# Performance work log

Measured on AMD Instinct MI355X. Metric: run time of the kernel, lower is better.

Reference implementation:

```python
import jax, jax.numpy as jnp
import numpy as np

NUM_HEADS = 16
NUM_KV_HEADS = 8
HEAD_DIM = 128
ROPE_THETA = 10000.0
SOFTCAP = 50.0


def rotate_half(x):
    x1, x2 = jnp.split(x, 2, axis=-1)
    return jnp.concatenate((-x2, x1), axis=-1)


def rope_cos_sin(seq_len):
    inv_freq = 1.0 / (ROPE_THETA ** (jnp.arange(0, HEAD_DIM, 2, dtype=jnp.float32) / HEAD_DIM))
    t = jnp.arange(seq_len, dtype=jnp.float32)
    freqs = t[:, None] * inv_freq[None, :]          # [S, D/2]
    emb = jnp.concatenate((freqs, freqs), axis=-1)  # [S, D]
    return jnp.cos(emb), jnp.sin(emb)


def setup_inputs() -> dict:
    key = jax.random.key(0)
    k1, k2, k3, k4, k5 = jax.random.split(key, 5)
    B, S, H = 2, 2048, 2048
    sc = 1.0 / np.sqrt(H)
    return {
        "hidden_states": jax.random.normal(k1, (B, S, H), dtype=jnp.float32),
        "Wq": jax.random.normal(k2, (H, NUM_HEADS * HEAD_DIM), dtype=jnp.float32) * sc,
        "Wk": jax.random.normal(k3, (H, NUM_KV_HEADS * HEAD_DIM), dtype=jnp.float32) * sc,
        "Wv": jax.random.normal(k4, (H, NUM_KV_HEADS * HEAD_DIM), dtype=jnp.float32) * sc,
        "Wo": jax.random.normal(k5, (NUM_HEADS * HEAD_DIM, H), dtype=jnp.float32) * sc,
    }


def reference(hidden_states, Wq, Wk, Wv, Wo):
    B, S, _ = hidden_states.shape
    groups = NUM_HEADS // NUM_KV_HEADS

    # projections -> [B, heads, S, D]
    q = (hidden_states @ Wq).reshape(B, S, NUM_HEADS, HEAD_DIM).transpose(0, 2, 1, 3)
    k = (hidden_states @ Wk).reshape(B, S, NUM_KV_HEADS, HEAD_DIM).transpose(0, 2, 1, 3)
    v = (hidden_states @ Wv).reshape(B, S, NUM_KV_HEADS, HEAD_DIM).transpose(0, 2, 1, 3)

    cos, sin = rope_cos_sin(S)  # [S, D], broadcast over (B, heads)
    q = q * cos + rotate_half(q) * sin
    k = k * cos + rotate_half(k) * sin

    # GQA: expand KV heads (repeat_interleave along head dim)
    k = jnp.repeat(k, groups, axis=1)
    v = jnp.repeat(v, groups, axis=1)

    scores = jnp.einsum('bhsd,bhtd->bhst', q, k) / np.sqrt(HEAD_DIM)
    scores = jnp.tanh(scores / SOFTCAP) * SOFTCAP  # Gemma logit softcapping
    weights = jax.nn.softmax(scores.astype(jnp.float32), axis=-1).astype(q.dtype)

    out = jnp.einsum('bhst,bhtd->bhsd', weights, v)
    out = out.transpose(0, 2, 1, 3).reshape(B, S, NUM_HEADS * HEAD_DIM)
    return out @ Wo
```

## Files before the change

### kernel.cpp

```cpp
#include <hip/hip_runtime.h>
#include <math.h>

typedef __bf16 bf16;
typedef __bf16 bf16x8 __attribute__((ext_vector_type(8)));
typedef __bf16 bf16x4 __attribute__((ext_vector_type(4)));
typedef float f32x2 __attribute__((ext_vector_type(2)));
typedef float f32x4 __attribute__((ext_vector_type(4)));
typedef float f32x16 __attribute__((ext_vector_type(16)));
typedef unsigned int uint;
typedef uint u32x4 __attribute__((ext_vector_type(4)));
typedef uint u32x2 __attribute__((ext_vector_type(2)));
typedef __bf16 bf16x8_a __attribute__((ext_vector_type(8), __may_alias__));
typedef uint u32x2_a __attribute__((ext_vector_type(2), __may_alias__));
typedef __bf16 bf16x4_a __attribute__((ext_vector_type(4), __may_alias__));
typedef __bf16 bf16_a __attribute__((__may_alias__));

constexpr int BATCH = 2;
constexpr int SEQ   = 2048;
constexpr int HID   = 2048;
constexpr int NHEAD = 16;
constexpr int NKV   = 8;
constexpr int HD    = 128;
constexpr int MROWS = BATCH * SEQ;

#define DEVINL __device__ __forceinline__

#define BAR()                                 \
  do {                                        \
    asm volatile("" ::: "memory");            \
    __builtin_amdgcn_s_barrier();             \
    asm volatile("" ::: "memory");            \
  } while (0)

#define WAITV(N) asm volatile("s_waitcnt vmcnt(" #N ")" ::: "memory")

DEVINL void async16(void* l, const void* g) {
  __builtin_amdgcn_global_load_lds((const __attribute__((address_space(1))) void*)g,
                                   (__attribute__((address_space(3))) void*)l, 16, 0, 0);
}

DEVINL f32x4 mfma16(bf16x8 a, bf16x8 b, f32x4 c) {
  return __builtin_amdgcn_mfma_f32_16x16x32_bf16(a, b, c, 0, 0, 0);
}
DEVINL f32x16 mfma32(bf16x8 a, bf16x8 b, f32x16 c) {
  return __builtin_amdgcn_mfma_f32_32x32x16_bf16(a, b, c, 0, 0, 0);
}

DEVINL f32x4 fzero4() { f32x4 z; z[0] = 0.f; z[1] = 0.f; z[2] = 0.f; z[3] = 0.f; return z; }

DEVINL float ex2(float x) {
#if __has_builtin(__builtin_amdgcn_exp2f)
  return __builtin_amdgcn_exp2f(x);
#else
  return __expf(x * 0.6931471805599453f);
#endif
}

DEVINL uint pkbf16(float lo, float hi) {
  unsigned short l = __builtin_bit_cast(unsigned short, (bf16)lo);
  unsigned short h = __builtin_bit_cast(unsigned short, (bf16)hi);
  return (uint)l | ((uint)h << 16);
}

DEVINL u32x2 pswap(uint a, uint b) {
#if __has_builtin(__builtin_amdgcn_permlane32_swap)
  return __builtin_amdgcn_permlane32_swap(a, b, false, false);
#else
  int hl = (int)((threadIdx.x >> 5) & 1);
  uint as = __shfl_xor(a, 32), bs = __shfl_xor(b, 32);
  u32x2 r;
  r[0] = hl ? bs : a;
  r[1] = hl ? b : as;
  return r;
#endif
}

__global__ __launch_bounds__(256) void prep(const float* __restrict__ X,
                                            const float* __restrict__ Wq,
                                            const float* __restrict__ Wk,
                                            const float* __restrict__ Wv,
                                            const float* __restrict__ Wo,
                                            bf16* __restrict__ Xb,
                                            bf16* __restrict__ WqT, bf16* __restrict__ WkT,
                                            bf16* __restrict__ WvT, bf16* __restrict__ WoT,
                                            float* __restrict__ ct, float* __restrict__ st) {
  const int tid = threadIdx.x;
  const int z = blockIdx.z;
  if (z == 4) {
    int idx = (blockIdx.y * 32 + blockIdx.x) * 256 + tid;
    if (idx < SEQ * 64) {
      int s = idx >> 6, d = idx & 63;
      float freq = powf(10000.0f, -(float)d * (1.0f / 64.0f));
      float a = (float)s * freq;
      ct[idx] = cosf(a);
      st[idx] = sinf(a);
    }
    return;
  }
  if (z == 5) {
    int j = (blockIdx.y * 32 + blockIdx.x) * 256 + tid;
#pragma unroll
    for (int it = 0; it < 8; it++) {
      int e = (it * 262144 + j) * 4;
      float4 v = *(const float4*)(X + e);
      bf16x4 o;
      o[0] = (bf16)v.x; o[1] = (bf16)v.y; o[2] = (bf16)v.z; o[3] = (bf16)v.w;
      *(bf16x4*)(Xb + e) = o;
    }
    return;
  }
  __shared__ bf16 t[64][65];
  const float* W; bf16* WT; int N;
  switch (z) {
    case 0: W = Wq; WT = WqT; N = 2048; break;
    case 1: W = Wk; WT = WkT; N = 1024; break;
    case 2: W = Wv; WT = WvT; N = 1024; break;
    default: W = Wo; WT = WoT; N = 2048; break;
  }
  int n0 = blockIdx.x * 64, k0 = blockIdx.y * 64;
  if (n0 >= N) return;
#pragma unroll
  for (int p = 0; p < 4; p++) {
    int r = (tid >> 4) + p * 16;
    int c4 = (tid & 15) * 4;
    float4 v = *(const float4*)(&W[(size_t)(k0 + r) * N + n0 + c4]);
    t[r][c4 + 0] = (bf16)v.x;
    t[r][c4 + 1] = (bf16)v.y;
    t[r][c4 + 2] = (bf16)v.z;
    t[r][c4 + 3] = (bf16)v.w;
  }
  __syncthreads();
#pragma unroll
  for (int p = 0; p < 4; p++) {
    int nr = (tid >> 4) + p * 16;
    int kb = (tid & 15) * 4;
    bf16x4 o;
    o[0] = t[kb + 0][nr];
    o[1] = t[kb + 1][nr];
    o[2] = t[kb + 2][nr];
    o[3] = t[kb + 3][nr];
    *(bf16x4_a*)(&WT[(size_t)(n0 + nr) * 2048 + k0 + kb]) = o;
  }
}

__global__ __launch_bounds__(256) void vtrans(const bf16* __restrict__ V, bf16* __restrict__ VT) {
  __shared__ bf16 t[64][65];
  int s0 = blockIdx.x * 64, d0 = blockIdx.y * 64;
  int bh = blockIdx.z, b = bh >> 3, kvh = bh & 7;
  for (int i = threadIdx.x; i < 4096; i += 256) {
    int r = i >> 6, c = i & 63;
    t[r][c] = V[(size_t)(b * SEQ + s0 + r) * (NKV * HD) + kvh * HD + d0 + c];
  }
  __syncthreads();
  for (int i = threadIdx.x; i < 4096; i += 256) {
    int r = i >> 6, c = i & 63;
    VT[((size_t)bh * HD + d0 + r) * SEQ + s0 + c] = t[c][r];
  }
}

__global__ __launch_bounds__(256) void gemmA(const bf16* __restrict__ A,
                                             const bf16* __restrict__ BT,
                                             bf16* __restrict__ C0, bf16* __restrict__ C1,
                                             bf16* __restrict__ C2, int K,
                                             const float* __restrict__ ct,
                                             const float* __restrict__ st) {
  __shared__ alignas(16) char ldsA[16384];
  __shared__ alignas(16) char ldsB[16384];
  const int tid = threadIdx.x, lane = tid & 63, w = tid >> 6;
  const int l15 = lane & 15, l4 = lane >> 4;
  const int gx = 32;
  const int nwg = gx * gridDim.y;
  int id = blockIdx.y * gx + blockIdx.x;
  id = (id & 7) * (nwg >> 3) + (id >> 3);
  const int row0 = (id / gx) * 128;
  const int col0 = (id % gx) * 128;

  f32x4 acc[2][8];
#pragma unroll
  for (int mt = 0; mt < 2; mt++)
#pragma unroll
    for (int nt = 0; nt < 8; nt++) acc[mt][nt] = fzero4();

  const bf16* Asrc = A + (size_t)row0 * K;
  const bf16* Bsrc = BT + (size_t)col0 * K;
  const int nk = K >> 6;

  for (int t = 0; t < nk; ++t) {
    const int k0 = t << 6;
    BAR();
#pragma unroll
    for (int j = 0; j < 4; j++) {
      int ci = j * 256 + tid;
      int r = ci >> 3, ps = ci & 7, ls = ps ^ (r & 7);
      async16(ldsA + ci * 16, Asrc + (size_t)r * K + k0 + ls * 8);
      async16(ldsB + ci * 16, Bsrc + (size_t)r * K + k0 + ls * 8);
    }
    WAITV(0);
    BAR();

    bf16x8 af[2][2];
#pragma unroll
    for (int mt = 0; mt < 2; mt++)
#pragma unroll
      for (int kc = 0; kc < 2; kc++) {
        int r = w * 32 + mt * 16 + l15;
        int off = ((r << 7) + ((kc * 4 + l4) << 4)) ^ ((r & 7) << 4);
        af[mt][kc] = *(const bf16x8_a*)(ldsA + off);
      }
#pragma unroll
    for (int nt = 0; nt < 8; nt++) {
#pragma unroll
      for (int kc = 0; kc < 2; kc++) {
        int c = nt * 16 + l15;
        int off = ((c << 7) + ((kc * 4 + l4) << 4)) ^ ((c & 7) << 4);
        bf16x8 bfr = *(const bf16x8_a*)(ldsB + off);
        acc[0][nt] = mfma16(af[0][kc], bfr, acc[0][nt]);
        acc[1][nt] = mfma16(af[1][kc], bfr, acc[1][nt]);
      }
    }
  }

#pragma unroll
  for (int mt = 0; mt < 2; mt++)
#pragma unroll
    for (int nt = 0; nt < 8; nt++)
#pragma unroll
      for (int rg = 0; rg < 4; rg++) {
        int row = row0 + w * 32 + mt * 16 + l4 * 4 + rg;
        int cl = col0 + nt * 16 + l15;
        float v = acc[mt][nt][rg];
        if (cl < 3072) {
          int s = row & (SEQ - 1);
          int ntp = (nt < 4) ? nt + 4 : nt - 4;
          float pv = (nt < 4) ? -acc[mt][ntp][rg] : acc[mt][ntp][rg];
          float cc = ct[s * 64 + (cl & 63)];
          float ss = st[s * 64 + (cl & 63)];
          v = fmaf(v, cc, pv * ss);
        }
        if (cl < 2048) {
          v *= 1.7677669529663689e-3f;
          C0[(size_t)row * 2048 + cl] = (bf16)v;
        } else if (cl < 3072) {
          C1[(size_t)row * 1024 + (cl - 2048)] = (bf16)v;
        } else {
          C2[(size_t)row * 1024 + (cl - 3072)] = (bf16)v;
        }
      }
}

__global__ __launch_bounds__(512, 2) void gemm2p(const bf16* __restrict__ A,
                                                 const bf16* __restrict__ BT,
                                                 float* __restrict__ C, int M, int N, int K) {
  __shared__ alignas(16) char ldsA[65536];
  __shared__ alignas(16) char ldsB[49152];
  const int tid = threadIdx.x, lane = tid & 63, w = tid >> 6;
  const int l15 = lane & 15, l4 = lane >> 4;
  const int wm = w >> 1, wn = w & 1;
  const int gx = gridDim.x;
  const int nwg = gx * gridDim.y;
  int id = blockIdx.y * gx + blockIdx.x;
  id = (id & 7) * (nwg >> 3) + (id >> 3);
  const int row0 = (id / gx) * 256;
  const int col0 = (id % gx) * 128;

  f32x4 acc[4][4];
#pragma unroll
  for (int mt = 0; mt < 4; mt++)
#pragma unroll
    for (int nt = 0; nt < 4; nt++) acc[mt][nt] = fzero4();

  const int rG0 = tid >> 3, sG0 = ((tid & 7) ^ (rG0 & 7)) * 8;
  const int ci1 = 512 + tid;
  const int rG1 = ci1 >> 3, sG1 = ((ci1 & 7) ^ (rG1 & 7)) * 8;
  const int dst0 = tid * 16, dst1 = (512 + tid) * 16;

  const bf16* Asrc = A + (size_t)row0 * K;
  const bf16* Bsrc = BT + (size_t)col0 * K;
  const int nk = K >> 6;

#define STG_A2(half, kt, buf)                                        \
  {                                                                  \
    char* d = ldsA + (buf) * 32768 + (half) * 16384;                 \
    const bf16* s = Asrc + (size_t)((half) * 128) * K + (kt) * 64;   \
    async16(d + dst0, s + (size_t)rG0 * K + sG0);                    \
    async16(d + dst1, s + (size_t)rG1 * K + sG1);                    \
  }
#define STG_B2(kt, buf)                                              \
  {                                                                  \
    char* d = ldsB + (buf) * 16384;                                  \
    const bf16* s = Bsrc + (kt) * 64;                                \
    async16(d + dst0, s + (size_t)rG0 * K + sG0);                    \
    async16(d + dst1, s + (size_t)rG1 * K + sG1);                    \
  }

  STG_B2(0, 0) STG_A2(0, 0, 0) STG_A2(1, 0, 0)
  STG_B2(1, 1) STG_A2(0, 1, 1) STG_A2(1, 1, 1)
  WAITV(6);
  BAR();

  bf16x8 af[8];
  bf16x8 bfr[8];

  for (int t = 0; t < nk; ++t) {
    const int abuf = t & 1;
    int bb = t % 3;
    const char* bA = ldsA + abuf * 32768 + (wm >> 1) * 16384;
    const char* bB = ldsB + bb * 16384;
    const bool s2 = (t + 2) < nk;
    int bb2 = bb + 2; if (bb2 >= 3) bb2 -= 3;

#pragma unroll
    for (int mt = 0; mt < 4; mt++)
#pragma unroll
      for (int kc = 0; kc < 2; kc++) {
        int r = (wm & 1) * 64 + mt * 16 + l15;
        int off = ((r << 7) + ((kc * 4 + l4) << 4)) ^ ((r & 7) << 4);
        af[mt * 2 + kc] = *(const bf16x8_a*)(bA + off);
      }
#pragma unroll
    for (int nt = 0; nt < 4; nt++)
#pragma unroll
      for (int kc = 0; kc < 2; kc++) {
        int c = wn * 16 + nt * 32 + l15;
        int off = ((c << 7) + ((kc * 4 + l4) << 4)) ^ ((c & 7) << 4);
        bfr[nt * 2 + kc] = *(const bf16x8_a*)(bB + off);
      }
    BAR();
    if (s2) { STG_B2(t + 2, bb2) STG_A2(0, t + 2, abuf) STG_A2(1, t + 2, abuf) }
    __builtin_amdgcn_s_setprio(1);
#pragma unroll
    for (int mt = 0; mt < 4; mt++)
#pragma unroll
      for (int nt = 0; nt < 4; nt++)
#pragma unroll
        for (int kc = 0; kc < 2; kc++)
          acc[mt][nt] = mfma16(af[mt * 2 + kc], bfr[nt * 2 + kc], acc[mt][nt]);
    __builtin_amdgcn_s_setprio(0);
    if (s2) { WAITV(6); } else { WAITV(0); }
    BAR();
  }
#undef STG_A2
#undef STG_B2

#pragma unroll
  for (int mt = 0; mt < 4; mt++)
#pragma unroll
    for (int nt = 0; nt < 4; nt++)
#pragma unroll
      for (int rg = 0; rg < 4; rg++) {
        int row = row0 + wm * 64 + mt * 16 + l4 * 4 + rg;
        int cl = col0 + wn * 16 + nt * 32 + l15;
        C[(size_t)row * N + cl] = acc[mt][nt][rg];
      }
}

__global__ __launch_bounds__(512, 2) void attn10(const bf16* __restrict__ Q,
                                                 const bf16* __restrict__ Kg,
                                                 const bf16* __restrict__ VTg,
                                                 bf16* __restrict__ O) {
  __shared__ alignas(16) char ldsK[49152];
  __shared__ alignas(16) char ldsV[49152];
  const int tid = threadIdx.x, lane = tid & 63, w = tid >> 6;
  const int l31 = lane & 31, hl = lane >> 5;

  const int nx = gridDim.x, ny = gridDim.y;
  const int nwg = nx * ny * gridDim.z;
  int id = (blockIdx.z * ny + blockIdx.y) * nx + blockIdx.x;
  id = (id & 7) * (nwg >> 3) + (id >> 3);
  const int qt = id % nx; id /= nx;
  const int h = id % ny; const int b = id / ny;
  const int kvh = h >> 1;
  const int qrow = b * SEQ + qt * 256 + w * 32 + l31;

  bf16x8 qf[8];
  const bf16* qp = Q + (size_t)qrow * (NHEAD * HD) + h * HD + hl * 8;
#pragma unroll
  for (int kc = 0; kc < 8; kc++) qf[kc] = *(const bf16x8_a*)(qp + kc * 16);

  f32x16 oT[4];
#pragma unroll
  for (int dt = 0; dt < 4; dt++)
#pragma unroll
    for (int r = 0; r < 16; r++) oT[dt][r] = 0.f;
  f32x2 ls2; ls2[0] = 0.f; ls2[1] = 0.f;

  const int rK = tid >> 4, sK = (tid & 15) ^ (rK & 15);
  const int rV = tid >> 3, sV = (tid & 7) ^ (rV & 7);
  const size_t koff0 = (size_t)(b * SEQ + rK) * (NKV * HD) + kvh * HD + sK * 8;
  const size_t voff0 = ((size_t)(b * NKV + kvh) * HD + rV) * SEQ + sV * 8;

  const float Ac = 72.13475204444817f;
  const float Bc = -24.044917348149389f;

  auto STAGE = [&](int buf, int t) {
    char* dK = ldsK + buf * 16384;
    char* dV = ldsV + buf * 16384;
    const bf16* ks = Kg + koff0 + (size_t)t * (64 * NKV * HD);
    const bf16* vs = VTg + voff0 + (size_t)t * 64;
    async16(dK + tid * 16, ks);
    async16(dK + (512 + tid) * 16, ks + (size_t)32 * (NKV * HD));
    async16(dV + tid * 16, vs);
    async16(dV + (512 + tid) * 16, vs + (size_t)64 * SEQ);
  };

  const int kvr0 = l31, kvr1 = 32 + l31;

#define QKT(SC, lKp)                                                     \
  do {                                                                   \
    _Pragma("unroll")                                                    \
    for (int r = 0; r < 16; r++) { (SC)[0][r] = 0.f; (SC)[1][r] = 0.f; } \
    _Pragma("unroll")                                                    \
    for (int kc = 0; kc < 8; kc++) {                                     \
      int slot = kc * 2 + hl;                                            \
      int off0 = (kvr0 << 8) | ((slot ^ (kvr0 & 15)) << 4);              \
      int off1 = (kvr1 << 8) | ((slot ^ (kvr1 & 15)) << 4);              \
      bf16x8 kf0 = *(const bf16x8_a*)((lKp) + off0);                     \
      bf16x8 kf1 = *(const bf16x8_a*)((lKp) + off1);                     \
      (SC)[0] = mfma32(kf0, qf[kc], (SC)[0]);                            \
      (SC)[1] = mfma32(kf1, qf[kc], (SC)[1]);                            \
    }                                                                    \
  } while (0)

#define SOFTMAX(SC, PB)                                                  \
  do {                                                                   \
    _Pragma("unroll")                                                    \
    for (int ntb = 0; ntb < 2; ntb++) {                                  \
      uint u[4][2];                                                      \
      _Pragma("unroll")                                                  \
      for (int r2 = 0; r2 < 8; r2++) {                                   \
        f32x2 z; z[0] = (SC)[ntb][2 * r2]; z[1] = (SC)[ntb][2 * r2 + 1]; \
        f32x2 z2 = z * z;                                                \
        f32x2 wv = z2 * Bc + Ac;                                         \
        f32x2 e = z * wv;                                                \
        float p0 = ex2(e[0]), p1 = ex2(e[1]);                            \
        ls2[0] += p0; ls2[1] += p1;                                      \
        u[r2 >> 1][r2 & 1] = pkbf16(p0, p1);                             \
      }                                                                  \
      _Pragma("unroll")                                                  \
      for (int sub = 0; sub < 2; sub++) {                                \
        u32x2 r0 = pswap(u[2 * sub][0], u[2 * sub + 1][0]);              \
        u32x2 r1 = pswap(u[2 * sub][1], u[2 * sub + 1][1]);              \
        u32x4 bu;                                                        \
        bu[0] = r0[0];                                                   \
        bu[1] = r1[0];                                                   \
        bu[2] = r0[1];                                                   \
        bu[3] = r1[1];                                                   \
        (PB)[ntb * 2 + sub] = __builtin_bit_cast(bf16x8, bu);            \
      }                                                                  \
    }                                                                    \
  } while (0)

#define PVACC(PB, lVp)                                                   \
  do {                                                                   \
    _Pragma("unroll")                                                    \
    for (int kvb = 0; kvb < 4; kvb++) {                                  \
      int slot = kvb * 2 + hl;                                           \
      _Pragma("unroll")                                                  \
      for (int dt = 0; dt < 4; dt++) {                                   \
        int d = dt * 32 + l31;                                           \
        int off = (d << 7) | ((slot ^ (d & 7)) << 4);                    \
        bf16x8 vf = *(const bf16x8_a*)((lVp) + off);                     \
        oT[dt] = mfma32(vf, (PB)[kvb], oT[dt]);                          \
      }                                                                  \
    }                                                                    \
  } while (0)

  constexpr int NT = SEQ / 64;
  STAGE(0, 0);
  STAGE(1, 1);
  WAITV(4);
  BAR();

  f32x16 scA[2], scB[2];
  bf16x8 pb[4];
  QKT(scA, ldsK);

  for (int it = 0; it < NT / 2; ++it) {
    const int t0 = 2 * it;
    {
      const int t = t0;
      BAR();
      if (t + 2 < NT) STAGE((t + 2) % 3, t + 2);
      SOFTMAX(scA, pb);
      if (t + 2 < NT) { WAITV(4); } else { WAITV(0); }
      BAR();
      __builtin_amdgcn_s_setprio(1);
      if (t + 1 < NT) QKT(scB, ldsK + ((t + 1) % 3) * 16384);
      PVACC(pb, ldsV + (t % 3) * 16384);
      __builtin_amdgcn_s_setprio(0);
    }
    {
      const int t = t0 + 1;
      BAR();
      if (t + 2 < NT) STAGE((t + 2) % 3, t + 2);
      SOFTMAX(scB, pb);
      if (t + 2 < NT) { WAITV(4); } else { WAITV(0); }
      BAR();
      __builtin_amdgcn_s_setprio(1);
      if (t + 1 < NT) QKT(scA, ldsK + ((t + 1) % 3) * 16384);
      PVACC(pb, ldsV + (t % 3) * 16384);
      __builtin_amdgcn_s_setprio(0);
    }
  }
#undef QKT
#undef SOFTMAX
#undef PVACC

  float lsum = ls2[0] + ls2[1];
  float lsf = lsum + __shfl_xor(lsum, 32);
  float inv = 1.0f / lsf;
  bf16* ob = O + (size_t)qrow * (NHEAD * HD) + h * HD;
#pragma unroll
  for (int dt = 0; dt < 4; dt++)
#pragma unroll
    for (int g = 0; g < 4; g++) {
      u32x2 pr;
      pr[0] = pkbf16(oT[dt][4 * g] * inv, oT[dt][4 * g + 1] * inv);
      pr[1] = pkbf16(oT[dt][4 * g + 2] * inv, oT[dt][4 * g + 3] * inv);
      *(u32x2_a*)(ob + dt * 32 + 8 * g + 4 * hl) = pr;
    }
}

extern "C" void kernel_launch(void* const* d_in, const int* in_sizes, int n_in,
                              void* d_out, int out_size, void* d_ws, size_t ws_size,
                              hipStream_t stream) {
  const float* X  = (const float*)d_in[0];
  const float* Wq = (const float*)d_in[1];
  const float* Wk = (const float*)d_in[2];
  const float* Wv = (const float*)d_in[3];
  const float* Wo = (const float*)d_in[4];
  float* out = (float*)d_out;

  char* ws = (char*)d_ws;
  size_t off = 0;
  auto alloc = [&](size_t bytes) {
    void* p = ws + off;
    off += (bytes + 255) & ~(size_t)255;
    return p;
  };
  bf16* Xb  = (bf16*)alloc((size_t)MROWS * HID * 2);
  bf16* WqT = (bf16*)alloc((size_t)2048 * 2048 * 2);
  bf16* WkT = (bf16*)alloc((size_t)1024 * 2048 * 2);
  bf16* WvT = (bf16*)alloc((size_t)1024 * 2048 * 2);
  bf16* WoT = (bf16*)alloc((size_t)2048 * 2048 * 2);
  bf16* Qb  = (bf16*)alloc((size_t)MROWS * 2048 * 2);
  bf16* Kb  = (bf16*)alloc((size_t)MROWS * 1024 * 2);
  bf16* Vb  = (bf16*)alloc((size_t)MROWS * 1024 * 2);
  bf16* VTb = (bf16*)alloc((size_t)16 * 128 * 2048 * 2);
  bf16* AOb = (bf16*)alloc((size_t)MROWS * 2048 * 2);
  float* ct = (float*)alloc((size_t)SEQ * 64 * 4);
  float* st = (float*)alloc((size_t)SEQ * 64 * 4);

  prep<<<dim3(32, 32, 6), 256, 0, stream>>>(X, Wq, Wk, Wv, Wo, Xb, WqT, WkT, WvT, WoT, ct, st);
  gemmA<<<dim3(32, 32), 256, 0, stream>>>(Xb, WqT, Qb, Kb, Vb, 2048, ct, st);
  vtrans<<<dim3(32, 2, 16), 256, 0, stream>>>(Vb, VTb);
  attn10<<<dim3(8, 16, 2), 512, 0, stream>>>(Qb, Kb, VTb, AOb);
  gemm2p<<<dim3(16, 16), 512, 0, stream>>>(AOb, WoT, out, MROWS, 2048, 2048);

  (void)in_sizes; (void)n_in; (void)out_size; (void)ws_size;
}
```

Before: 263.6 us.

## Rewrite QKV projection GEMM with 256x128 tiles and multi-stage async LDS pipeline

Replaces the single-buffered 128x128 QKV GEMM with a 512-thread, 256x128-tile kernel that prefetches two K-steps ahead (double-buffered A, triple-buffered B) and raises wave priority around the MFMA block. The aim is to overlap global-to-LDS loads with MFMA work instead of waiting on every tile, and to reuse more data per load. The fused RoPE epilogue is remapped to the new wave layout, with rotate-half pairs found via nt^2. It uses much more LDS and more registers, and halves the grid, which may limit occupancy.

Result: faster. 250.1 us (-5.1%).

```diff
diff --git a/kernel.cpp b/kernel.cpp
--- a/kernel.cpp
+++ b/kernel.cpp
@@ -158,84 +158,118 @@
   }
 }
 
-__global__ __launch_bounds__(256) void gemmA(const bf16* __restrict__ A,
-                                             const bf16* __restrict__ BT,
-                                             bf16* __restrict__ C0, bf16* __restrict__ C1,
-                                             bf16* __restrict__ C2, int K,
-                                             const float* __restrict__ ct,
-                                             const float* __restrict__ st) {
-  __shared__ alignas(16) char ldsA[16384];
-  __shared__ alignas(16) char ldsB[16384];
+__global__ __launch_bounds__(512, 2) void gemmB(const bf16* __restrict__ A,
+                                                const bf16* __restrict__ BT,
+                                                bf16* __restrict__ C0, bf16* __restrict__ C1,
+                                                bf16* __restrict__ C2, int K,
+                                                const float* __restrict__ ct,
+                                                const float* __restrict__ st) {
+  __shared__ alignas(16) char ldsA[65536];
+  __shared__ alignas(16) char ldsB[49152];
   const int tid = threadIdx.x, lane = tid & 63, w = tid >> 6;
   const int l15 = lane & 15, l4 = lane >> 4;
+  const int wm = w >> 1, wn = w & 1;
   const int gx = 32;
   const int nwg = gx * gridDim.y;
   int id = blockIdx.y * gx + blockIdx.x;
   id = (id & 7) * (nwg >> 3) + (id >> 3);
-  const int row0 = (id / gx) * 128;
+  const int row0 = (id / gx) * 256;
   const int col0 = (id % gx) * 128;
 
-  f32x4 acc[2][8];
-#pragma unroll
-  for (int mt = 0; mt < 2; mt++)
-#pragma unroll
-    for (int nt = 0; nt < 8; nt++) acc[mt][nt] = fzero4();
+  f32x4 acc[4][4];
+#pragma unroll
+  for (int mt = 0; mt < 4; mt++)
+#pragma unroll
+    for (int nt = 0; nt < 4; nt++) acc[mt][nt] = fzero4();
+
+  const int rG0 = tid >> 3, sG0 = ((tid & 7) ^ (rG0 & 7)) * 8;
+  const int ci1 = 512 + tid;
+  const int rG1 = ci1 >> 3, sG1 = ((ci1 & 7) ^ (rG1 & 7)) * 8;
+  const int dst0 = tid * 16, dst1 = (512 + tid) * 16;
 
   const bf16* Asrc = A + (size_t)row0 * K;
   const bf16* Bsrc = BT + (size_t)col0 * K;
   const int nk = K >> 6;
 
+#define STG_A2(half, kt, buf)                                        \
+  {                                                                  \
+    char* d = ldsA + (buf) * 32768 + (half) * 16384;                 \
+    const bf16* s = Asrc + (size_t)((half) * 128) * K + (kt) * 64;   \
+    async16(d + dst0, s + (size_t)rG0 * K + sG0);                    \
+    async16(d + dst1, s + (size_t)rG1 * K + sG1);                    \
+  }
+#define STG_B2(kt, buf)                                              \
+  {                                                                  \
+    char* d = ldsB + (buf) * 16384;                                  \
+    const bf16* s = Bsrc + (kt) * 64;                                \
+    async16(d + dst0, s + (size_t)rG0 * K + sG0);                    \
+    async16(d + dst1, s + (size_t)rG1 * K + sG1);                    \
+  }
+
+  STG_B2(0, 0) STG_A2(0, 0, 0) STG_A2(1, 0, 0)
+  STG_B2(1, 1) STG_A2(0, 1, 1) STG_A2(1, 1, 1)
+  WAITV(6);
+  BAR();
+
+  bf16x8 af[8];
+  bf16x8 bfr[8];
+
   for (int t = 0; t < nk; ++t) {
-    const int k0 = t << 6;
+    const int abuf = t & 1;
+    int bb = t % 3;
+    const char* bA = ldsA + abuf * 32768 + (wm >> 1) * 16384;
+    const char* bB = ldsB + bb * 16384;
+    const bool s2 = (t + 2) < nk;
+    int bb2 = bb + 2; if (bb2 >= 3) bb2 -= 3;
+
+#pragma unroll
+    for (int mt = 0; mt < 4; mt++)
+#pragma unroll
+      for (int kc = 0; kc < 2; kc++) {
+        int r = (wm & 1) * 64 + mt * 16 + l15;
+        int off = ((r << 7) + ((kc * 4 + l4) << 4)) ^ ((r & 7) << 4);
+        af[mt * 2 + kc] = *(const bf16x8_a*)(bA + off);
+      }
+#pragma unroll
+    for (int nt = 0; nt < 4; nt++)
+#pragma unroll
+      for (int kc = 0; kc < 2; kc++) {
+        int c = wn * 16 + nt * 32 + l15;
+        int off = ((c << 7) + ((kc * 4 + l4) << 4)) ^ ((c & 7) << 4);
+        bfr[nt * 2 + kc] = *(const bf16x8_a*)(bB + off);
+      }
     BAR();
-#pragma unroll
-    for (int j = 0; j < 4; j++) {
-      int ci = j * 256 + tid;
-      int r = ci >> 3, ps = ci & 7, ls = ps ^ (r & 7);
-      async16(ldsA + ci * 16, Asrc + (size_t)r * K + k0 + ls * 8);
-      async16(ldsB + ci * 16, Bsrc + (size_t)r * K + k0 + ls * 8);
-    }
-    WAITV(0);
+    if (s2) { STG_B2(t + 2, bb2) STG_A2(0, t + 2, abuf) STG_A2(1, t + 2, abuf) }
+    __builtin_amdgcn_s_setprio(1);
+#pragma unroll
+    for (int mt = 0; mt < 4; mt++)
+#pragma unroll
+      for (int nt = 0; nt < 4; nt++)
+#pragma unroll
+        for (int kc = 0; kc < 2; kc++)
+          acc[mt][nt] = mfma16(af[mt * 2 + kc], bfr[nt * 2 + kc], acc[mt][nt]);
+    __builtin_amdgcn_s_setprio(0);
+    if (s2) { WAITV(6); } else { WAITV(0); }
     BAR();
-
-    bf16x8 af[2][2];
-#pragma unroll
-    for (int mt = 0; mt < 2; mt++)
-#pragma unroll
-      for (int kc = 0; kc < 2; kc++) {
-        int r = w * 32 + mt * 16 + l15;
-        int off = ((r << 7) + ((kc * 4 + l4) << 4)) ^ ((r & 7) << 4);
-        af[mt][kc] = *(const bf16x8_a*)(ldsA + off);
-      }
-#pragma unroll
-    for (int nt = 0; nt < 8; nt++) {
-#pragma unroll
-      for (int kc = 0; kc < 2; kc++) {
-        int c = nt * 16 + l15;
-        int off = ((c << 7) + ((kc * 4 + l4) << 4)) ^ ((c & 7) << 4);
-        bf16x8 bfr = *(const bf16x8_a*)(ldsB + off);
-        acc[0][nt] = mfma16(af[0][kc], bfr, acc[0][nt]);
-        acc[1][nt] = mfma16(af[1][kc], bfr, acc[1][nt]);
-      }
-    }
-  }
-
-#pragma unroll
-  for (int mt = 0; mt < 2; mt++)
-#pragma unroll
-    for (int nt = 0; nt < 8; nt++)
+  }
+#undef STG_A2
+#undef STG_B2
+
+#pragma unroll
+  for (int mt = 0; mt < 4; mt++)
+#pragma unroll
+    for (int nt = 0; nt < 4; nt++)
 #pragma unroll
       for (int rg = 0; rg < 4; rg++) {
-        int row = row0 + w * 32 + mt * 16 + l4 * 4 + rg;
-        int cl = col0 + nt * 16 + l15;
+        int row = row0 + wm * 64 + mt * 16 + l4 * 4 + rg;
+        int cl = col0 + wn * 16 + nt * 32 + l15;
         float v = acc[mt][nt][rg];
         if (cl < 3072) {
           int s = row & (SEQ - 1);
-          int ntp = (nt < 4) ? nt + 4 : nt - 4;
-          float pv = (nt < 4) ? -acc[mt][ntp][rg] : acc[mt][ntp][rg];
+          float pv = acc[mt][nt ^ 2][rg];
           float cc = ct[s * 64 + (cl & 63)];
           float ss = st[s * 64 + (cl & 63)];
-          v = fmaf(v, cc, pv * ss);
+          v = (nt < 2) ? fmaf(v, cc, -pv * ss) : fmaf(v, cc, pv * ss);
         }
         if (cl < 2048) {
           v *= 1.7677669529663689e-3f;
@@ -552,7 +586,7 @@
   float* st = (float*)alloc((size_t)SEQ * 64 * 4);
 
   prep<<<dim3(32, 32, 6), 256, 0, stream>>>(X, Wq, Wk, Wv, Wo, Xb, WqT, WkT, WvT, WoT, ct, st);
-  gemmA<<<dim3(32, 32), 256, 0, stream>>>(Xb, WqT, Qb, Kb, Vb, 2048, ct, st);
+  gemmB<<<dim3(32, 16), 512, 0, stream>>>(Xb, WqT, Qb, Kb, Vb, 2048, ct, st);
   vtrans<<<dim3(32, 2, 16), 256, 0, stream>>>(Vb, VTb);
   attn10<<<dim3(8, 16, 2), 512, 0, stream>>>(Qb, Kb, VTb, AOb);
   gemm2p<<<dim3(16, 16), 512, 0, stream>>>(AOb, WoT, out, MROWS, 2048, 2048);
```
